# Kernel optimization log

Measured on AMD Instinct MI355X. Metric: run time of the kernel, lower is better.

## Reference

```python
import jax, jax.numpy as jnp
import numpy as np

B, TX, TY = 1024, 512, 32
NA, NS = 64, 128
VIN, VOUT = 64, 32


def setup_inputs() -> dict:
    key = jax.random.key(0)
    ks = jax.random.split(key, 19)
    g = lambda k, shape: (jax.random.normal(k, shape, dtype=jnp.float32) * 0.1)
    return {
        'X': jax.random.normal(ks[0], (B, TX, VIN), dtype=jnp.float32),
        # bidirectional encoder LSTM (torch gate order i,f,g,o)
        'Wih_f': g(ks[1], (4 * NA, VIN)), 'Whh_f': g(ks[2], (4 * NA, NA)),
        'bih_f': g(ks[3], (4 * NA,)), 'bhh_f': g(ks[4], (4 * NA,)),
        'Wih_b': g(ks[5], (4 * NA, VIN)), 'Whh_b': g(ks[6], (4 * NA, NA)),
        'bih_b': g(ks[7], (4 * NA,)), 'bhh_b': g(ks[8], (4 * NA,)),
        # decoder LSTM (input n_s, hidden n_s)
        'Wih_p': g(ks[9], (4 * NS, NS)), 'Whh_p': g(ks[10], (4 * NS, NS)),
        'bih_p': g(ks[11], (4 * NS,)), 'bhh_p': g(ks[12], (4 * NS,)),
        # attention MLP and output head
        'W1': g(ks[13], (10, 2 * NS)), 'b1': g(ks[14], (10,)),
        'W2': g(ks[15], (1, 10)), 'b2': g(ks[16], (1,)),
        'W3': g(ks[17], (VOUT, 2 * NA)), 'b3': g(ks[18], (VOUT,)),
    }


def _lstm_cell(x, h, c, Wih, Whh, b):
    z = x @ Wih.T + h @ Whh.T + b
    i, f, g, o = jnp.split(z, 4, axis=-1)
    c = jax.nn.sigmoid(f) * c + jax.nn.sigmoid(i) * jnp.tanh(g)
    h = jax.nn.sigmoid(o) * jnp.tanh(c)
    return h, c


def _lstm_scan(x, Wih, Whh, b):
    # x: (B, T, I) -> outputs (B, T, H)
    bs = x.shape[0]
    h0 = jnp.zeros((bs, Wih.shape[0] // 4), x.dtype)
    def step(carry, xt):
        h, c = _lstm_cell(xt, carry[0], carry[1], Wih, Whh, b)
        return (h, c), h
    _, ys = jax.lax.scan(step, (h0, h0), jnp.swapaxes(x, 0, 1))
    return jnp.swapaxes(ys, 0, 1)


def reference(X, Wih_f, Whh_f, bih_f, bhh_f, Wih_b, Whh_b, bih_b, bhh_b,
              Wih_p, Whh_p, bih_p, bhh_p, W1, b1, W2, b2, W3, b3):
    bs = X.shape[0]
    # bidirectional encoder: forward pass + reversed pass, concat features
    fwd = _lstm_scan(X, Wih_f, Whh_f, bih_f + bhh_f)
    bwd = _lstm_scan(X[:, ::-1], Wih_b, Whh_b, bih_b + bhh_b)[:, ::-1]
    pre_out = jnp.concatenate([fwd, bwd], axis=-1)  # (B, TX, 2*NA) == (B, TX, NS)

    bp = bih_p + bhh_p

    def dec_step(carry, _):
        s, c = carry  # each (B, NS)
        # additive attention: repeat state over TX, concat with encoder outputs
        state_rep = jnp.broadcast_to(s[:, None, :], pre_out.shape)  # (B, TX, NS)
        comb = jnp.concatenate([state_rep, pre_out], axis=-1)       # (B, TX, 2*NS)
        e = jnp.tanh(comb @ W1.T + b1)
        e = jax.nn.relu(e @ W2.T + b2)                               # (B, TX, 1)
        alphas = jax.nn.softmax(e, axis=1)
        context = jnp.sum(alphas * pre_out, axis=1)                  # (B, NS)
        s, c = _lstm_cell(context, s, c, Wih_p, Whh_p, bp)
        # NOTE: original applies Softmax(dim=1) to (1, B, V) -> softmax over BATCH; faithful here
        out = jax.nn.softmax(s @ W3.T + b3, axis=0)                  # (B, VOUT)
        return (s, c), out

    s0 = jnp.zeros((bs, NS), X.dtype)
    _, outs = jax.lax.scan(dec_step, (s0, s0), None, length=TY)      # (TY, B, VOUT)
    return jnp.swapaxes(outs, 0, 1)                                   # (B, TY, VOUT)
```

## Files before the change

### kernel.cpp

```cpp
#include <hip/hip_runtime.h>
#include <stdint.h>

#define B_    1024
#define TX_   512
#define TY_   32
#define NA_   64
#define NS_   128
#define VIN_  64
#define VOUT_ 32

typedef short v8s __attribute__((ext_vector_type(8)));
typedef float v4f __attribute__((ext_vector_type(4)));

__device__ __forceinline__ unsigned short f2bf(float f) {
  union { float f; uint32_t u; } v; v.f = f;
  return (unsigned short)((v.u + 0x7fffu + ((v.u >> 16) & 1u)) >> 16);
}
__device__ __forceinline__ float bflo(uint32_t p) { union { uint32_t u; float f; } v; v.u = p << 16; return v.f; }
__device__ __forceinline__ float bfhi(uint32_t p) { union { uint32_t u; float f; } v; v.u = p & 0xffff0000u; return v.f; }
__device__ __forceinline__ float sigm(float x)   { return 1.0f / (1.0f + __expf(-x)); }
__device__ __forceinline__ float tanh_f(float x) { return 1.0f - 2.0f / (__expf(2.0f * x) + 1.0f); }

__global__ __launch_bounds__(256) void k_prep(const float* __restrict__ Wih_p,
                                              const float* __restrict__ Whh_p,
                                              unsigned short* __restrict__ Wsw) {
  int i = blockIdx.x * 256 + threadIdx.x;
  int j = i & 7, lane = (i >> 3) & 63, f = i >> 9;
  int r = (f >> 3) * 16 + (lane & 15);
  int c = (f & 7) * 32 + (lane >> 4) * 8 + j;
  float w = (c < 128) ? Wih_p[r * 128 + c] : Whh_p[r * 128 + (c - 128)];
  Wsw[i] = f2bf(w);
}

__global__ __launch_bounds__(256) void k_enc(
    const float* __restrict__ X,
    const float* __restrict__ Wih_f, const float* __restrict__ Whh_f,
    const float* __restrict__ bih_f, const float* __restrict__ bhh_f,
    const float* __restrict__ Wih_b, const float* __restrict__ Whh_b,
    const float* __restrict__ bih_b, const float* __restrict__ bhh_b,
    unsigned short* __restrict__ pre16)
{
  const int tid = threadIdx.x, lane = tid & 63, wv = tid >> 6;
  const int dir = blockIdx.x & 1, b0 = (blockIdx.x >> 1) * 16;
  const int n = lane & 15, q = lane >> 4, hs = wv * 16;
  const float* Wih = dir ? Wih_b : Wih_f;
  const float* Whh = dir ? Whh_b : Whh_f;
  const float* bih = dir ? bih_b : bih_f;
  const float* bhh = dir ? bhh_b : bhh_f;

  __shared__ __align__(16) unsigned short hl[16 * 72];

  v8s wx[4][2], wh[4][2];
  float bias[4];
#pragma unroll
  for (int g = 0; g < 4; ++g) {
    int row = g * 64 + hs + n;
    bias[g] = bih[row] + bhh[row];
#pragma unroll
    for (int kt = 0; kt < 2; ++kt) {
      const float* pi = Wih + row * 64 + kt * 32 + q * 8;
      const float* ph = Whh + row * 64 + kt * 32 + q * 8;
      v8s a, bb;
#pragma unroll
      for (int j = 0; j < 8; ++j) { a[j] = (short)f2bf(pi[j]); bb[j] = (short)f2bf(ph[j]); }
      wx[g][kt] = a; wh[g][kt] = bb;
    }
  }
  for (int i = tid; i < 16 * 36; i += 256) ((uint32_t*)hl)[i] = 0u;

  float c[4] = {0.f, 0.f, 0.f, 0.f};
  const float* xrow = X + (size_t)(b0 + n) * (TX_ * VIN_) + q * 8;
  int t0 = dir ? (TX_ - 1) : 0;
  float4 pf0 = *(const float4*)(xrow + t0 * VIN_ + 0);
  float4 pf1 = *(const float4*)(xrow + t0 * VIN_ + 4);
  float4 pf2 = *(const float4*)(xrow + t0 * VIN_ + 32);
  float4 pf3 = *(const float4*)(xrow + t0 * VIN_ + 36);
  __syncthreads();

  for (int t = 0; t < TX_; ++t) {
    v8s xa0, xa1;
    xa0[0]=(short)f2bf(pf0.x); xa0[1]=(short)f2bf(pf0.y); xa0[2]=(short)f2bf(pf0.z); xa0[3]=(short)f2bf(pf0.w);
    xa0[4]=(short)f2bf(pf1.x); xa0[5]=(short)f2bf(pf1.y); xa0[6]=(short)f2bf(pf1.z); xa0[7]=(short)f2bf(pf1.w);
    xa1[0]=(short)f2bf(pf2.x); xa1[1]=(short)f2bf(pf2.y); xa1[2]=(short)f2bf(pf2.z); xa1[3]=(short)f2bf(pf2.w);
    xa1[4]=(short)f2bf(pf3.x); xa1[5]=(short)f2bf(pf3.y); xa1[6]=(short)f2bf(pf3.z); xa1[7]=(short)f2bf(pf3.w);
    int tn = (t + 1 < TX_) ? t + 1 : t;
    int ti = dir ? (TX_ - 1 - tn) : tn;
    pf0 = *(const float4*)(xrow + ti * VIN_ + 0);
    pf1 = *(const float4*)(xrow + ti * VIN_ + 4);
    pf2 = *(const float4*)(xrow + ti * VIN_ + 32);
    pf3 = *(const float4*)(xrow + ti * VIN_ + 36);

    v8s ha0 = *(const v8s*)((const char*)hl + (lane & 15) * 144 + q * 16);
    v8s ha1 = *(const v8s*)((const char*)hl + (lane & 15) * 144 + 64 + q * 16);
    v4f acc[4];
#pragma unroll
    for (int g = 0; g < 4; ++g) {
      v4f a = {bias[g], bias[g], bias[g], bias[g]};
      a = __builtin_amdgcn_mfma_f32_16x16x32_bf16(xa0, wx[g][0], a, 0, 0, 0);
      a = __builtin_amdgcn_mfma_f32_16x16x32_bf16(xa1, wx[g][1], a, 0, 0, 0);
      a = __builtin_amdgcn_mfma_f32_16x16x32_bf16(ha0, wh[g][0], a, 0, 0, 0);
      a = __builtin_amdgcn_mfma_f32_16x16x32_bf16(ha1, wh[g][1], a, 0, 0, 0);
      acc[g] = a;
    }
    __syncthreads();
    int t_out = dir ? (TX_ - 1 - t) : t;
#pragma unroll
    for (int r = 0; r < 4; ++r) {
      float cc = sigm(acc[1][r]) * c[r] + sigm(acc[0][r]) * tanh_f(acc[2][r]);
      c[r] = cc;
      float h = sigm(acc[3][r]) * tanh_f(cc);
      int m = q * 4 + r;
      unsigned short hb = f2bf(h);
      *((unsigned short*)((char*)hl + m * 144) + hs + n) = hb;
      pre16[((size_t)(b0 + m) * TX_ + t_out) * NS_ + dir * 64 + hs + n] = hb;
    }
    __syncthreads();
  }
}

#define PO_   0
#define PP_   139264
#define EA_   149504
#define RED_  151552
#define ZB_   155648
#define SL_   157696
#define XPK_  158208
#define CX_   158720
#define QV_   159232
#define RR_   159296
#define DSM_  159360

__global__ __launch_bounds__(512) __attribute__((amdgpu_waves_per_eu(2, 2))) void k_dec(
    const unsigned short* __restrict__ pre16,
    const unsigned short* __restrict__ Wsw,
    const float* __restrict__ W1, const float* __restrict__ b1,
    const float* __restrict__ W2, const float* __restrict__ b2,
    const float* __restrict__ W3, const float* __restrict__ b3,
    const float* __restrict__ bih_p, const float* __restrict__ bhh_p,
    float* __restrict__ Lg)
{
  extern __shared__ char smem[];
  char* po = smem + PO_;
  unsigned short* P = (unsigned short*)(smem + PP_);
  float* ea  = (float*)(smem + EA_);
  float* red = (float*)(smem + RED_);
  float* zbf = (float*)(smem + ZB_);
  float* sl  = (float*)(smem + SL_);
  uint32_t* xpk = (uint32_t*)(smem + XPK_);
  float* qv  = (float*)(smem + QV_);
  float* rr  = (float*)(smem + RR_);

  const int b = blockIdx.x, tid = threadIdx.x, lane = tid & 63, wv = tid >> 6;

  {
    const uint4* src = (const uint4*)((const char*)pre16 + (size_t)b * (TX_ * NS_ * 2));
    for (int i = tid; i < TX_ * 16; i += 512) {
      int t = i >> 4, d8 = i & 15;
      *(uint4*)(po + t * 272 + d8 * 16) = src[i];
    }
  }
  if (tid < 128) { sl[tid] = 0.f; xpk[tid] = 0u; }
  if (tid < 16) qv[tid] = 0.f;
  float* w1p = (float*)(smem + RED_);
  for (int i = tid; i < 1280; i += 512) { int g = i >> 7, k = i & 127; w1p[i] = W1[g * 256 + 128 + k]; }
  __syncthreads();
  {
    int t = tid;
    float a[10];
#pragma unroll
    for (int g = 0; g < 10; ++g) a[g] = b1[g];
    for (int k2 = 0; k2 < 64; ++k2) {
      uint32_t pr = *(const uint32_t*)(po + t * 272 + k2 * 4);
      float lo = bflo(pr), hi = bfhi(pr);
#pragma unroll
      for (int g = 0; g < 10; ++g) a[g] += lo * w1p[g * 128 + 2 * k2] + hi * w1p[g * 128 + 2 * k2 + 1];
    }
#pragma unroll
    for (int g = 0; g < 10; ++g) P[t * 10 + g] = f2bf(a[g]);
  }

  v8s wfr[4][8];
#pragma unroll
  for (int nt = 0; nt < 4; ++nt)
#pragma unroll
    for (int kt = 0; kt < 8; ++kt)
      wfr[nt][kt] = ((const v8s*)Wsw)[((wv * 4 + nt) * 8 + kt) * 64 + lane];
  float bp4[4];
#pragma unroll
  for (int nt = 0; nt < 4; ++nt) {
    int r = wv * 64 + nt * 16 + (lane & 15);
    bp4[nt] = bih_p[r] + bhh_p[r];
  }
  float creg = 0.f;
  __syncthreads();

  for (int ty = 0; ty < TY_; ++ty) {
    {
      float qr[10];
#pragma unroll
      for (int g = 0; g < 10; ++g) qr[g] = qv[g];
      const uint32_t* Pt = (const uint32_t*)(const void*)P + tid * 5;
      float acc = b2[0];
#pragma unroll
      for (int i = 0; i < 5; ++i) {
        uint32_t pr = Pt[i];
        acc += W2[2 * i]     * tanh_f(bflo(pr) + qr[2 * i]);
        acc += W2[2 * i + 1] * tanh_f(bfhi(pr) + qr[2 * i + 1]);
      }
      float e = fmaxf(acc, 0.f);
      float m = e;
#pragma unroll
      for (int off = 1; off < 64; off <<= 1) m = fmaxf(m, __shfl_xor(m, off));
      if (lane == 0) rr[wv] = m;
      __syncthreads();
      float mx = rr[0];
#pragma unroll
      for (int w = 1; w < 8; ++w) mx = fmaxf(mx, rr[w]);
      float p = __expf(e - mx);
      float s = p;
#pragma unroll
      for (int off = 1; off < 64; off <<= 1) s += __shfl_xor(s, off);
      if (lane == 0) rr[8 + wv] = s;
      __syncthreads();
      float S = rr[8];
#pragma unroll
      for (int w = 1; w < 8; ++w) S += rr[8 + w];
      ea[tid] = p / S;
    }
    __syncthreads();
    {
      int d8 = lane & 15, g4 = lane >> 4, tg = wv * 4 + g4;
      float p8[8];
#pragma unroll
      for (int j = 0; j < 8; ++j) p8[j] = 0.f;
      for (int i = 0; i < 16; ++i) {
        int t = i * 32 + tg;
        float al = ea[t];
        uint4 pk = *(const uint4*)(po + t * 272 + d8 * 16);
        p8[0] += al * bflo(pk.x); p8[1] += al * bfhi(pk.x);
        p8[2] += al * bflo(pk.y); p8[3] += al * bfhi(pk.y);
        p8[4] += al * bflo(pk.z); p8[5] += al * bfhi(pk.z);
        p8[6] += al * bflo(pk.w); p8[7] += al * bfhi(pk.w);
      }
#pragma unroll
      for (int off = 16; off < 64; off <<= 1) {
#pragma unroll
        for (int j = 0; j < 8; ++j) p8[j] += __shfl_xor(p8[j], off);
      }
      if (lane < 16) {
        float4* dst = (float4*)&red[wv * 128 + d8 * 8];
        dst[0] = make_float4(p8[0], p8[1], p8[2], p8[3]);
        dst[1] = make_float4(p8[4], p8[5], p8[6], p8[7]);
      }
    }
    __syncthreads();
    if (tid < 64) {
      float v0 = 0.f, v1 = 0.f;
#pragma unroll
      for (int w = 0; w < 8; ++w) { v0 += red[w * 128 + 2 * tid]; v1 += red[w * 128 + 2 * tid + 1]; }
      xpk[tid] = ((uint32_t)f2bf(v1) << 16) | (uint32_t)f2bf(v0);
    }
    __syncthreads();
    {
      const int q = lane >> 4;
      v8s zv;
#pragma unroll
      for (int j = 0; j < 8; ++j) zv[j] = 0;
      const bool a0 = (lane & 15) == 0;
      const char* xb = (const char*)xpk + q * 16;
      v8s xa[8];
#pragma unroll
      for (int kt = 0; kt < 8; ++kt)
        xa[kt] = a0 ? *(const v8s*)(xb + kt * 64) : zv;
#pragma unroll
      for (int nt = 0; nt < 4; ++nt) {
        v4f a = {0.f, 0.f, 0.f, 0.f};
#pragma unroll
        for (int kt = 0; kt < 8; ++kt)
          a = __builtin_amdgcn_mfma_f32_16x16x32_bf16(xa[kt], wfr[nt][kt], a, 0, 0, 0);
        if (lane < 16) zbf[wv * 64 + nt * 16 + lane] = a[0] + bp4[nt];
      }
    }
    __syncthreads();
    if (tid < 128) {
      float zi = zbf[tid], zf = zbf[128 + tid], zg = zbf[256 + tid], zo = zbf[384 + tid];
      creg = sigm(zf) * creg + sigm(zi) * tanh_f(zg);
      sl[tid] = sigm(zo) * tanh_f(creg);
    }
    __syncthreads();
    if (wv == 0) {
      xpk[64 + lane] = ((uint32_t)f2bf(sl[2 * lane + 1]) << 16) | (uint32_t)f2bf(sl[2 * lane]);
    } else if (wv == 1) {
      float p10[10];
      float s0 = sl[lane], s1 = sl[lane + 64];
#pragma unroll
      for (int g = 0; g < 10; ++g) p10[g] = s0 * W1[g * 256 + lane] + s1 * W1[g * 256 + 64 + lane];
#pragma unroll
      for (int off = 1; off < 64; off <<= 1) {
#pragma unroll
        for (int g = 0; g < 10; ++g) p10[g] += __shfl_xor(p10[g], off);
      }
      if (lane < 10) qv[lane] = p10[lane];
    } else if (wv < 6) {
      int v = (tid - 128) >> 3, kg = tid & 7;
      float a = 0.f;
#pragma unroll
      for (int k = kg * 16; k < kg * 16 + 16; ++k) a += sl[k] * W3[v * 128 + k];
      red[v * 8 + kg] = a;
    }
    __syncthreads();
    if (tid < 32) {
      float a = b3[tid];
#pragma unroll
      for (int i = 0; i < 8; ++i) a += red[tid * 8 + i];
      Lg[(size_t)ty * (B_ * VOUT_) + b * VOUT_ + tid] = a;
    }
    __syncthreads();
  }
}

__global__ __launch_bounds__(256) void k_red(const float* __restrict__ Lg, float2* __restrict__ MS) {
  int ty = blockIdx.x >> 5, v = blockIdx.x & 31;
  const float* src = Lg + (size_t)ty * (B_ * VOUT_) + v;
  int tid = threadIdx.x, lane = tid & 63, wv = tid >> 6;
  __shared__ float r8[8];
  float m = -3.4e38f;
  for (int bb = tid; bb < B_; bb += 256) m = fmaxf(m, src[(size_t)bb * VOUT_]);
#pragma unroll
  for (int off = 1; off < 64; off <<= 1) m = fmaxf(m, __shfl_xor(m, off));
  if (lane == 0) r8[wv] = m;
  __syncthreads();
  float mx = fmaxf(fmaxf(r8[0], r8[1]), fmaxf(r8[2], r8[3]));
  float s = 0.f;
  for (int bb = tid; bb < B_; bb += 256) s += __expf(src[(size_t)bb * VOUT_] - mx);
#pragma unroll
  for (int off = 1; off < 64; off <<= 1) s += __shfl_xor(s, off);
  __syncthreads();
  if (lane == 0) r8[4 + wv] = s;
  __syncthreads();
  if (tid == 0) MS[blockIdx.x] = make_float2(mx, r8[4] + r8[5] + r8[6] + r8[7]);
}

__global__ __launch_bounds__(256) void k_out(const float* __restrict__ Lg,
                                             const float2* __restrict__ MS,
                                             float* __restrict__ out) {
  int i = blockIdx.x * 256 + threadIdx.x;
  int ty = i >> 15, b = (i >> 5) & 1023, v = i & 31;
  float2 ms = MS[ty * 32 + v];
  out[(size_t)b * (TY_ * VOUT_) + ty * VOUT_ + v] = __expf(Lg[i] - ms.x) / ms.y;
}

#define WS_PRE 0
#define WS_WSW 134217728
#define WS_LG  134479872
#define WS_MS  138674176

extern "C" void kernel_launch(void* const* d_in, const int* in_sizes, int n_in,
                              void* d_out, int out_size, void* d_ws, size_t ws_size,
                              hipStream_t stream) {
  const float* X     = (const float*)d_in[0];
  const float* Wih_f = (const float*)d_in[1];
  const float* Whh_f = (const float*)d_in[2];
  const float* bih_f = (const float*)d_in[3];
  const float* bhh_f = (const float*)d_in[4];
  const float* Wih_b = (const float*)d_in[5];
  const float* Whh_b = (const float*)d_in[6];
  const float* bih_b = (const float*)d_in[7];
  const float* bhh_b = (const float*)d_in[8];
  const float* Wih_p = (const float*)d_in[9];
  const float* Whh_p = (const float*)d_in[10];
  const float* bih_p = (const float*)d_in[11];
  const float* bhh_p = (const float*)d_in[12];
  const float* W1    = (const float*)d_in[13];
  const float* b1    = (const float*)d_in[14];
  const float* W2    = (const float*)d_in[15];
  const float* b2    = (const float*)d_in[16];
  const float* W3    = (const float*)d_in[17];
  const float* b3    = (const float*)d_in[18];

  char* ws = (char*)d_ws;
  unsigned short* pre16 = (unsigned short*)(ws + WS_PRE);
  unsigned short* Wsw   = (unsigned short*)(ws + WS_WSW);
  float*          Lg    = (float*)(ws + WS_LG);
  float2*         MS    = (float2*)(ws + WS_MS);

  (void)hipFuncSetAttribute((const void*)k_dec, hipFuncAttributeMaxDynamicSharedMemorySize, DSM_);

  k_prep<<<512, 256, 0, stream>>>(Wih_p, Whh_p, Wsw);
  k_enc<<<128, 256, 0, stream>>>(X, Wih_f, Whh_f, bih_f, bhh_f,
                                 Wih_b, Whh_b, bih_b, bhh_b, pre16);
  k_dec<<<1024, 512, DSM_, stream>>>(pre16, Wsw, W1, b1, W2, b2, W3, b3,
                                     bih_p, bhh_p, Lg);
  k_red<<<1024, 256, 0, stream>>>(Lg, MS);
  k_out<<<4096, 256, 0, stream>>>(Lg, MS, (float*)d_out);
}
```

Baseline: 1.702 ms.

## Double decoder block to 1024 threads and split per-step work across thread pairs

The decoder kernel now runs 16 waves per batch block instead of 8. The attention-score precompute and the per-step score evaluation are split across thread pairs and combined with a lane shuffle. The gate MFMA work is spread over twice as many waves, each holding half the weight fragments, and the trailing barrier of each step is dropped. The intent is more latency hiding and shorter serial chains in this latency-bound recurrent loop, at the cost of a tighter per-wave register budget and extra shuffle and barrier traffic across more waves.

```diff
diff --git a/kernel.cpp b/kernel.cpp
--- a/kernel.cpp
+++ b/kernel.cpp
@@ -125,12 +125,11 @@
 #define ZB_   155648
 #define SL_   157696
 #define XPK_  158208
-#define CX_   158720
-#define QV_   159232
-#define RR_   159296
+#define RR_   158720
+#define QV_   158848
 #define DSM_  159360
 
-__global__ __launch_bounds__(512) __attribute__((amdgpu_waves_per_eu(2, 2))) void k_dec(
+__global__ __launch_bounds__(1024) __attribute__((amdgpu_waves_per_eu(4, 4))) void k_dec(
     const unsigned short* __restrict__ pre16,
     const unsigned short* __restrict__ Wsw,
     const float* __restrict__ W1, const float* __restrict__ b1,
@@ -147,14 +146,14 @@
   float* zbf = (float*)(smem + ZB_);
   float* sl  = (float*)(smem + SL_);
   uint32_t* xpk = (uint32_t*)(smem + XPK_);
+  float* rr  = (float*)(smem + RR_);
   float* qv  = (float*)(smem + QV_);
-  float* rr  = (float*)(smem + RR_);
 
   const int b = blockIdx.x, tid = threadIdx.x, lane = tid & 63, wv = tid >> 6;
 
   {
     const uint4* src = (const uint4*)((const char*)pre16 + (size_t)b * (TX_ * NS_ * 2));
-    for (int i = tid; i < TX_ * 16; i += 512) {
+    for (int i = tid; i < TX_ * 16; i += 1024) {
       int t = i >> 4, d8 = i & 15;
       *(uint4*)(po + t * 272 + d8 * 16) = src[i];
     }
@@ -162,51 +161,54 @@
   if (tid < 128) { sl[tid] = 0.f; xpk[tid] = 0u; }
   if (tid < 16) qv[tid] = 0.f;
   float* w1p = (float*)(smem + RED_);
-  for (int i = tid; i < 1280; i += 512) { int g = i >> 7, k = i & 127; w1p[i] = W1[g * 256 + 128 + k]; }
+  for (int i = tid; i < 1280; i += 1024) { int g = i >> 7, k = i & 127; w1p[i] = W1[g * 256 + 128 + k]; }
   __syncthreads();
   {
-    int t = tid;
+    int t = tid >> 1, h = tid & 1;
     float a[10];
 #pragma unroll
-    for (int g = 0; g < 10; ++g) a[g] = b1[g];
-    for (int k2 = 0; k2 < 64; ++k2) {
+    for (int g = 0; g < 10; ++g) a[g] = h ? 0.f : b1[g];
+    for (int k2 = h * 32; k2 < h * 32 + 32; ++k2) {
       uint32_t pr = *(const uint32_t*)(po + t * 272 + k2 * 4);
       float lo = bflo(pr), hi = bfhi(pr);
 #pragma unroll
       for (int g = 0; g < 10; ++g) a[g] += lo * w1p[g * 128 + 2 * k2] + hi * w1p[g * 128 + 2 * k2 + 1];
     }
 #pragma unroll
-    for (int g = 0; g < 10; ++g) P[t * 10 + g] = f2bf(a[g]);
-  }
-
-  v8s wfr[4][8];
-#pragma unroll
-  for (int nt = 0; nt < 4; ++nt)
+    for (int g = 0; g < 10; ++g) a[g] += __shfl_xor(a[g], 1);
+    if (!h) {
+#pragma unroll
+      for (int g = 0; g < 10; ++g) P[t * 10 + g] = f2bf(a[g]);
+    }
+  }
+
+  v8s wfr[2][8];
+#pragma unroll
+  for (int nt = 0; nt < 2; ++nt)
 #pragma unroll
     for (int kt = 0; kt < 8; ++kt)
-      wfr[nt][kt] = ((const v8s*)Wsw)[((wv * 4 + nt) * 8 + kt) * 64 + lane];
-  float bp4[4];
-#pragma unroll
-  for (int nt = 0; nt < 4; ++nt) {
-    int r = wv * 64 + nt * 16 + (lane & 15);
-    bp4[nt] = bih_p[r] + bhh_p[r];
+      wfr[nt][kt] = ((const v8s*)Wsw)[((wv * 2 + nt) * 8 + kt) * 64 + lane];
+  float bp2[2];
+#pragma unroll
+  for (int nt = 0; nt < 2; ++nt) {
+    int r = wv * 32 + nt * 16 + (lane & 15);
+    bp2[nt] = bih_p[r] + bhh_p[r];
   }
   float creg = 0.f;
   __syncthreads();
 
   for (int ty = 0; ty < TY_; ++ty) {
     {
-      float qr[10];
-#pragma unroll
-      for (int g = 0; g < 10; ++g) qr[g] = qv[g];
-      const uint32_t* Pt = (const uint32_t*)(const void*)P + tid * 5;
-      float acc = b2[0];
+      int t = tid >> 1, h = tid & 1;
+      const uint32_t* Pt = (const uint32_t*)(const void*)P + t * 5;
+      float acc = h ? 0.f : b2[0];
 #pragma unroll
       for (int i = 0; i < 5; ++i) {
         uint32_t pr = Pt[i];
-        acc += W2[2 * i]     * tanh_f(bflo(pr) + qr[2 * i]);
-        acc += W2[2 * i + 1] * tanh_f(bfhi(pr) + qr[2 * i + 1]);
-      }
+        float pv = h ? bfhi(pr) : bflo(pr);
+        acc += W2[2 * i + h] * tanh_f(pv + qv[2 * i + h]);
+      }
+      acc += __shfl_xor(acc, 1);
       float e = fmaxf(acc, 0.f);
       float m = e;
 #pragma unroll
@@ -215,20 +217,21 @@
       __syncthreads();
       float mx = rr[0];
 #pragma unroll
-      for (int w = 1; w < 8; ++w) mx = fmaxf(mx, rr[w]);
+      for (int w = 1; w < 16; ++w) mx = fmaxf(mx, rr[w]);
       float p = __expf(e - mx);
-      float s = p;
+      float ps = h ? 0.f : p;
+      float s = ps;
 #pragma unroll
       for (int off = 1; off < 64; off <<= 1) s += __shfl_xor(s, off);
-      if (lane == 0) rr[8 + wv] = s;
+      if (lane == 0) rr[16 + wv] = s;
       __syncthreads();
-      float S = rr[8];
-#pragma unroll
-      for (int w = 1; w < 8; ++w) S += rr[8 + w];
-      ea[tid] = p / S;
-    }
-    __syncthreads();
-    {
+      float S = rr[16];
+#pragma unroll
+      for (int w = 1; w < 16; ++w) S += rr[16 + w];
+      if (!h) ea[t] = p / S;
+    }
+    __syncthreads();
+    if (wv < 8) {
       int d8 = lane & 15, g4 = lane >> 4, tg = wv * 4 + g4;
       float p8[8];
 #pragma unroll
@@ -273,12 +276,12 @@
       for (int kt = 0; kt < 8; ++kt)
         xa[kt] = a0 ? *(const v8s*)(xb + kt * 64) : zv;
 #pragma unroll
-      for (int nt = 0; nt < 4; ++nt) {
+      for (int nt = 0; nt < 2; ++nt) {
         v4f a = {0.f, 0.f, 0.f, 0.f};
 #pragma unroll
         for (int kt = 0; kt < 8; ++kt)
           a = __builtin_amdgcn_mfma_f32_16x16x32_bf16(xa[kt], wfr[nt][kt], a, 0, 0, 0);
-        if (lane < 16) zbf[wv * 64 + nt * 16 + lane] = a[0] + bp4[nt];
+        if (lane < 16) zbf[wv * 32 + nt * 16 + lane] = a[0] + bp2[nt];
       }
     }
     __syncthreads();
@@ -315,7 +318,6 @@
       for (int i = 0; i < 8; ++i) a += red[tid * 8 + i];
       Lg[(size_t)ty * (B_ * VOUT_) + b * VOUT_ + tid] = a;
     }
-    __syncthreads();
   }
 }
 
@@ -389,8 +391,8 @@
   k_prep<<<512, 256, 0, stream>>>(Wih_p, Whh_p, Wsw);
   k_enc<<<128, 256, 0, stream>>>(X, Wih_f, Whh_f, bih_f, bhh_f,
                                  Wih_b, Whh_b, bih_b, bhh_b, pre16);
-  k_dec<<<1024, 512, DSM_, stream>>>(pre16, Wsw, W1, b1, W2, b2, W3, b3,
-                                     bih_p, bhh_p, Lg);
+  k_dec<<<1024, 1024, DSM_, stream>>>(pre16, Wsw, W1, b1, W2, b2, W3, b3,
+                                      bih_p, bhh_p, Lg);
   k_red<<<1024, 256, 0, stream>>>(Lg, MS);
   k_out<<<4096, 256, 0, stream>>>(Lg, MS, (float*)d_out);
 }
```

New measurement: 3.289 ms. 1.93x slower.
